# Kernel tuning notes

Measured on AMD Instinct MI355X. Metric: run time of the kernel, lower is better.

Reference implementation:

```python
import jax, jax.numpy as jnp
import numpy as np
from jax import lax

B, L, D_MODEL = 4, 1024, 512
D_STATE, D_CONV, D_INNER = 16, 4, 2 * D_MODEL


def setup_inputs() -> dict:
    key = jax.random.key(0)
    ks = jax.random.split(key, 8)
    s = 0.02
    x = jax.random.normal(ks[0], (B, L, D_MODEL), dtype=jnp.float32)
    W_in = jax.random.normal(ks[1], (D_MODEL, 2 * D_INNER), dtype=jnp.float32) * s
    conv_w = jax.random.normal(ks[2], (D_INNER, 1, D_CONV), dtype=jnp.float32) * s  # OIH, depthwise
    conv_b = jnp.zeros((D_INNER,), jnp.float32)
    W_x = jax.random.normal(ks[3], (D_INNER, 2 * D_STATE), dtype=jnp.float32) * s
    W_dt = jax.random.normal(ks[4], (D_INNER, D_INNER), dtype=jnp.float32) * s
    b_dt = jnp.zeros((D_INNER,), jnp.float32)
    # A_log = -logspace(log10(0.001), log10(1.0), d_state); used directly as A in the scan
    A_log = -jnp.logspace(np.log10(1e-3), 0.0, D_STATE, dtype=jnp.float32)
    D_skip = jnp.ones((D_INNER,), jnp.float32) * 0.1
    W_out = jax.random.normal(ks[5], (D_INNER, D_MODEL), dtype=jnp.float32) * s
    gamma = jnp.ones((D_MODEL,), jnp.float32)
    beta = jnp.zeros((D_MODEL,), jnp.float32)
    return dict(x=x, W_in=W_in, conv_w=conv_w, conv_b=conv_b, W_x=W_x, W_dt=W_dt,
                b_dt=b_dt, A_log=A_log, D_skip=D_skip, W_out=W_out, gamma=gamma, beta=beta)


def _mamba_forward(x, W_in, conv_w, conv_b, W_x, W_dt, b_dt, A_log, D_skip, W_out, gamma, beta):
    x = jnp.clip(x, -10.0, 10.0)
    x_and_res = x @ W_in                                  # [B, L, 2*d_inner]
    xp, res = jnp.split(x_and_res, 2, axis=-1)
    # Depthwise causal conv1d: torch pads d_conv-1 both sides then slices [:L] -> left-pad only.
    xt = jnp.transpose(xp, (0, 2, 1))                     # [B, d_inner, L]
    xc = lax.conv_general_dilated(xt, conv_w, window_strides=(1,),
                                  padding=[(D_CONV - 1, 0)],
                                  dimension_numbers=('NCH', 'OIH', 'NCH'),
                                  feature_group_count=D_INNER)
    xc = xc + conv_b[None, :, None]
    xc = jax.nn.silu(jnp.transpose(xc, (0, 2, 1)))        # [B, L, d_inner]
    ssm = xc @ W_x                                        # [B, L, 2*d_state]
    Bm, Cm = jnp.split(ssm, 2, axis=-1)                   # each [B, L, d_state]
    delta = xc @ W_dt + b_dt                              # [B, L, d_inner] (no softplus in source)

    # Selective scan over time (sequential recurrence)
    def step(h, inp):
        u_t, d_t, B_t, C_t = inp                          # [B,I], [B,I], [B,S], [B,S]
        dA = jnp.exp(jnp.clip(d_t[:, :, None] * A_log, -5.0, 5.0))   # [B, I, S]
        h = dA * h + (d_t[:, :, None] * B_t[:, None, :]) * u_t[:, :, None]
        y = jnp.einsum('bis,bs->bi', h, C_t)
        return h, y

    tm = lambda a: jnp.swapaxes(a, 0, 1)                  # time-major
    h0 = jnp.zeros((x.shape[0], D_INNER, D_STATE), xc.dtype)
    _, ys = lax.scan(step, h0, (tm(xc), tm(delta), tm(Bm), tm(Cm)))
    y = jnp.swapaxes(ys, 0, 1) + xc * D_skip              # D skip connection

    y = y * jax.nn.silu(res)                              # gating
    out = y @ W_out
    r = out + x                                           # residual
    mu = jnp.mean(r, axis=-1, keepdims=True)
    var = jnp.var(r, axis=-1, keepdims=True)
    return gamma * (r - mu) / jnp.sqrt(var + 1e-5) + beta


def reference(x, W_in, conv_w, conv_b, W_x, W_dt, b_dt, A_log, D_skip, W_out, gamma, beta):
    return _mamba_forward(x, W_in, conv_w, conv_b, W_x, W_dt, b_dt, A_log, D_skip, W_out, gamma, beta)
```

## Files before the change

kernel.cpp:

```cpp
#include <hip/hip_runtime.h>
#include <hip/hip_bf16.h>

typedef __hip_bfloat16 bf16;
typedef unsigned short ushort_t;
typedef unsigned int uint_t;
typedef __attribute__((ext_vector_type(8))) __bf16 bf16x8;
typedef __attribute__((ext_vector_type(8))) ushort_t u16x8;
typedef __attribute__((ext_vector_type(4))) ushort_t u16x4;
typedef __attribute__((ext_vector_type(4))) float f32x4;

#define BB 4
#define LL 1024
#define DM 512
#define DS 16
#define DI 1024
#define ROWS 4096
#define NC 64
#define CT 16

__device__ __forceinline__ float b2f(bf16 v) { return __bfloat162float(v); }

__device__ __forceinline__ float load_flag(const void* src, int i, int isbf)
{
    return isbf ? b2f(((const bf16*)src)[i]) : ((const float*)src)[i];
}

__device__ __forceinline__ ushort_t f2b_bits(float v)
{
    bf16 t = __float2bfloat16(v);
    return *(ushort_t*)&t;
}

__device__ __forceinline__ float bits2f(ushort_t u)
{
    uint_t w = ((uint_t)u) << 16;
    return __uint_as_float(w);
}

__device__ __forceinline__ int detect_local(const ushort_t* wdt)
{
    __shared__ int bad;
    if (threadIdx.x == 0) bad = 0;
    __syncthreads();
    ushort_t u = wdt[threadIdx.x & 255];
    if (((u >> 7) & 0xFF) >= 127) atomicAdd(&bad, 1);
    __syncthreads();
    return (bad <= 8) ? 1 : 0;
}

__global__ __launch_bounds__(256)
void prep_all(const void* x, const void* Win, const void* Wdt, const void* Wx,
              const void* Wout, const void* cw, const void* cb, const void* Alog,
              const void* Dsk, const void* gam, const void* bet, const void* bdtin,
              bf16* __restrict__ xbf, bf16* __restrict__ WtIn,
              bf16* __restrict__ WtDt, bf16* __restrict__ WtSsm,
              bf16* __restrict__ WtOut,
              float* __restrict__ ccw, float* __restrict__ ccb,
              float* __restrict__ cAlg, float* __restrict__ cDsk,
              float* __restrict__ cgam, float* __restrict__ cbet,
              float* __restrict__ bdt)
{
    const int isbf = detect_local((const ushort_t*)Wdt);
    int blk = blockIdx.x;

    if (blk < 2048) {
        int idx = blk * 256 + threadIdx.x;
        float v[4];
        if (isbf) {
            uint2 raw = ((const uint2*)x)[idx];
            v[0] = __uint_as_float(raw.x << 16);
            v[1] = __uint_as_float(raw.x & 0xFFFF0000u);
            v[2] = __uint_as_float(raw.y << 16);
            v[3] = __uint_as_float(raw.y & 0xFFFF0000u);
        } else {
            float4 raw = ((const float4*)x)[idx];
            v[0] = raw.x; v[1] = raw.y; v[2] = raw.z; v[3] = raw.w;
        }
        uint_t b0, b1;
        b0 = f2b_bits(fminf(fmaxf(v[0], -10.f), 10.f))
           | ((uint_t)f2b_bits(fminf(fmaxf(v[1], -10.f), 10.f)) << 16);
        b1 = f2b_bits(fminf(fmaxf(v[2], -10.f), 10.f))
           | ((uint_t)f2b_bits(fminf(fmaxf(v[3], -10.f), 10.f)) << 16);
        uint2 ow; ow.x = b0; ow.y = b1;
        ((uint2*)xbf)[idx] = ow;
    } else if (blk < 4640) {
        int tb = blk - 2048;
        const void* src; bf16* dst; int K, Nsrc, tpr;
        if (tb < 1024)      { src = Win;  dst = WtIn;  K = 512;  Nsrc = 2048; tpr = 64; }
        else if (tb < 2048) { tb -= 1024; src = Wdt;  dst = WtDt;  K = 1024; Nsrc = 1024; tpr = 32; }
        else if (tb < 2080) { tb -= 2048; src = Wx;   dst = WtSsm; K = 1024; Nsrc = 32;   tpr = 1; }
        else                { tb -= 2080; src = Wout; dst = WtOut; K = 1024; Nsrc = 512;  tpr = 16; }
        int k0 = (tb / tpr) * 32, n0 = (tb % tpr) * 32;

        __shared__ float tile[32][33];
        int tx = threadIdx.x & 31, ty = threadIdx.x >> 5;
        #pragma unroll
        for (int j = 0; j < 4; ++j)
            tile[ty + 8 * j][tx] = load_flag(src, (k0 + ty + 8 * j) * Nsrc + n0 + tx, isbf);
        __syncthreads();
        #pragma unroll
        for (int j = 0; j < 4; ++j)
            dst[(size_t)(n0 + ty + 8 * j) * K + k0 + tx] = __float2bfloat16(tile[tx][ty + 8 * j]);
    } else {
        int i = (blk - 4640) * 256 + threadIdx.x;
        if (i < 4096)        ccw[i] = load_flag(cw, i, isbf);
        else if (i < 5120)   ccb[i - 4096] = load_flag(cb, i - 4096, isbf);
        else if (i < 5136)   cAlg[i - 5120] = load_flag(Alog, i - 5120, isbf);
        else if (i < 6160)   cDsk[i - 5136] = load_flag(Dsk, i - 5136, isbf);
        else if (i < 6672)   cgam[i - 6160] = load_flag(gam, i - 6160, isbf);
        else if (i < 7184)   cbet[i - 6672] = load_flag(bet, i - 6672, isbf);
        else if (i < 8208)   bdt[i - 7184] = load_flag(bdtin, i - 7184, isbf);
        else if (i < 40976)  (WtSsm + 32 * 1024)[i - 8208] = __float2bfloat16(0.f);
    }
}

__device__ __forceinline__ void gload16(const bf16* g, ushort_t* l)
{
    __builtin_amdgcn_global_load_lds(
        (const __attribute__((address_space(1))) void*)g,
        (__attribute__((address_space(3))) void*)l, 16, 0, 0);
}

template <int TM, int TN, bool OBF, bool OT>
__global__ __launch_bounds__(256)
void gemm_mfma(const bf16* __restrict__ A, const bf16* __restrict__ Bt,
               const float* __restrict__ bias, void* __restrict__ Cv,
               int M, int N, int K)
{
    constexpr int MI = TM / 32, NJ = TN / 32;
    constexpr int NQA = TM * 8 / 256;
    constexpr int NQB = TN * 8 / 256;
    __shared__ ushort_t As[TM * 64];
    __shared__ ushort_t Bs[TN * 64];

    const int tid = threadIdx.x;
    const int lane = tid & 63;
    const int w = tid >> 6;
    const int wr = w >> 1, wc = w & 1;
    const int m0 = blockIdx.y * TM;
    const int n0 = blockIdx.x * TN;

    const bf16* gA[NQA]; ushort_t* lA[NQA];
    #pragma unroll
    for (int q = 0; q < NQA; ++q) {
        int p = q * 256 + tid;
        int row = p >> 3, kc = ((p & 7) - row) & 7;
        gA[q] = A + (size_t)(m0 + row) * K + kc * 8;
        lA[q] = &As[(q * 256 + w * 64) * 8];
    }
    const bf16* gB[NQB]; ushort_t* lB[NQB];
    #pragma unroll
    for (int q = 0; q < NQB; ++q) {
        int p = q * 256 + tid;
        int row = p >> 3, kc = ((p & 7) - row) & 7;
        gB[q] = Bt + (size_t)(n0 + row) * K + kc * 8;
        lB[q] = &Bs[(q * 256 + w * 64) * 8];
    }

    f32x4 acc[MI][NJ];
    #pragma unroll
    for (int i = 0; i < MI; ++i)
        #pragma unroll
        for (int j = 0; j < NJ; ++j)
            acc[i][j] = (f32x4){0.f, 0.f, 0.f, 0.f};

    const int ko = lane >> 4;
    const int ml = lane & 15;

    for (int k0 = 0; k0 < K; k0 += 64) {
        #pragma unroll
        for (int q = 0; q < NQA; ++q) gload16(gA[q] + k0, lA[q]);
        #pragma unroll
        for (int q = 0; q < NQB; ++q) gload16(gB[q] + k0, lB[q]);
        __syncthreads();

        #pragma unroll
        for (int half = 0; half < 2; ++half) {
            bf16x8 af[MI], bfr[NJ];
            #pragma unroll
            for (int i = 0; i < MI; ++i) {
                int m = wr * (TM / 2) + i * 16 + ml;
                af[i] = *(const bf16x8*)&As[(m * 8 + ((half * 4 + ko + m) & 7)) * 8];
            }
            #pragma unroll
            for (int j = 0; j < NJ; ++j) {
                int n = wc * (TN / 2) + j * 16 + ml;
                bfr[j] = *(const bf16x8*)&Bs[(n * 8 + ((half * 4 + ko + n) & 7)) * 8];
            }
            #pragma unroll
            for (int i = 0; i < MI; ++i)
                #pragma unroll
                for (int j = 0; j < NJ; ++j)
                    acc[i][j] = __builtin_amdgcn_mfma_f32_16x16x32_bf16(
                        af[i], bfr[j], acc[i][j], 0, 0, 0);
        }
        __syncthreads();
    }

    const int rq = lane >> 4;
    #pragma unroll
    for (int j = 0; j < NJ; ++j) {
        int n = n0 + wc * (TN / 2) + j * 16 + ml;
        float bv = bias ? bias[n] : 0.f;
        #pragma unroll
        for (int i = 0; i < MI; ++i) {
            int mb = m0 + wr * (TM / 2) + i * 16 + rq * 4;
            if (OT) {
                u16x4 pk;
                #pragma unroll
                for (int r = 0; r < 4; ++r)
                    pk[r] = f2b_bits(acc[i][j][r] + bv);
                *(u16x4*)((ushort_t*)Cv + (size_t)n * M + mb) = pk;
            } else {
                #pragma unroll
                for (int r = 0; r < 4; ++r) {
                    float v = acc[i][j][r] + bv;
                    if (OBF) ((bf16*)Cv)[(size_t)(mb + r) * N + n] = __float2bfloat16(v);
                    else     ((float*)Cv)[(size_t)(mb + r) * N + n] = v;
                }
            }
        }
    }
}

__global__ __launch_bounds__(256)
void conv_silu(const bf16* __restrict__ xrbT, const float* __restrict__ cw,
               const float* __restrict__ cb, bf16* __restrict__ xcT,
               bf16* __restrict__ xc)
{
    __shared__ ushort_t tile[64 * 72];
    const int blk = blockIdx.x;
    const int ch0 = (blk & 15) * 64;
    const int T0b = (blk >> 4) * 64;
    const int lc = threadIdx.x >> 2, tg = threadIdx.x & 3;
    const int i = ch0 + lc;
    const int T0 = T0b + tg * 16;

    const ushort_t* base = (const ushort_t*)xrbT + (size_t)i * ROWS + T0;
    u16x8 m0 = *(const u16x8*)base;
    u16x8 m1 = *(const u16x8*)(base + 8);
    u16x8 pv = {0, 0, 0, 0, 0, 0, 0, 0};
    if ((T0 & (LL - 1)) != 0) pv = *(const u16x8*)(base - 8);

    float4 w = ((const float4*)cw)[i];
    float bs = cb[i];
    float xm3 = bits2f(pv[5]), xm2 = bits2f(pv[6]), xm1 = bits2f(pv[7]);
    u16x8 o0, o1;
    #pragma unroll
    for (int tt = 0; tt < 16; ++tt) {
        float x0 = bits2f(tt < 8 ? m0[tt] : m1[tt - 8]);
        float acc = bs;
        acc = fmaf(xm3, w.x, acc);
        acc = fmaf(xm2, w.y, acc);
        acc = fmaf(xm1, w.z, acc);
        acc = fmaf(x0,  w.w, acc);
        ushort_t ob = f2b_bits(acc / (1.f + __expf(-acc)));
        if (tt < 8) o0[tt] = ob; else o1[tt - 8] = ob;
        xm3 = xm2; xm2 = xm1; xm1 = x0;
    }
    ushort_t* dt = (ushort_t*)xcT + (size_t)i * ROWS + T0;
    *(u16x8*)dt = o0;
    *(u16x8*)(dt + 8) = o1;
    *(u16x8*)&tile[lc * 72 + tg * 16] = o0;
    *(u16x8*)&tile[lc * 72 + tg * 16 + 8] = o1;
    __syncthreads();
    const int lt = threadIdx.x >> 2, cg = threadIdx.x & 3;
    u16x8 q0, q1;
    #pragma unroll
    for (int j = 0; j < 8; ++j) q0[j] = tile[(cg * 16 + j) * 72 + lt];
    #pragma unroll
    for (int j = 8; j < 16; ++j) q1[j - 8] = tile[(cg * 16 + j) * 72 + lt];
    ushort_t* wp = (ushort_t*)xc + (size_t)(T0b + lt) * DI + ch0 + cg * 16;
    *(u16x8*)wp = q0;
    *(u16x8*)(wp + 8) = q1;
}

__global__ __launch_bounds__(1024)
void scan_fused(const bf16* __restrict__ xcT, const bf16* __restrict__ dT,
                const bf16* __restrict__ ssm, const bf16* __restrict__ xrbT,
                const float* __restrict__ A_log, const float* __restrict__ Dskip,
                bf16* __restrict__ ybf)
{
    __shared__ uint_t lsum[DS * NC * 16];

    const int tid = threadIdx.x;
    const int b = blockIdx.x >> 6;
    const int ch0 = (blockIdx.x & 63) << 4;
    const int chl = tid & 15;
    const int c = tid >> 4;
    const int i = ch0 + chl;
    const size_t tb = (size_t)b * LL + c * CT;

    float a[DS];
    #pragma unroll
    for (int s = 0; s < DS; ++s) {
        uint_t bits = (uint_t)__builtin_amdgcn_readfirstlane((int)__float_as_uint(A_log[s]));
        a[s] = __uint_as_float(bits);
    }

    const u16x8* dp = (const u16x8*)((const ushort_t*)dT + (size_t)i * ROWS + tb);
    const u16x8* up = (const u16x8*)((const ushort_t*)xcT + (size_t)i * ROWS + tb);
    const u16x8* rp = (const u16x8*)((const ushort_t*)xrbT + (size_t)(1024 + i) * ROWS + tb);

    float h[DS] = {};
    float p[DS];
    #pragma unroll
    for (int s = 0; s < DS; ++s) p[s] = 1.f;

    #pragma unroll
    for (int half = 0; half < 2; ++half) {
        u16x8 dv8 = dp[half];
        u16x8 uv8 = up[half];
        #pragma unroll
        for (int t = 0; t < 8; ++t) {
            float dv = bits2f(dv8[t]);
            float uv = bits2f(uv8[t]);
            float du = dv * uv;
            const u16x8* sp = (const u16x8*)((const ushort_t*)ssm + (tb + half * 8 + t) * 64);
            u16x8 B0 = sp[0], B1 = sp[1];
            #pragma unroll
            for (int s = 0; s < DS; ++s) {
                float e = fminf(fmaxf(dv * a[s], -5.f), 5.f);
                float dA = __expf(e);
                float Bv = bits2f(s < 8 ? B0[s] : B1[s - 8]);
                h[s] = fmaf(dA, h[s], du * Bv);
                p[s] *= dA;
            }
        }
    }
    #pragma unroll
    for (int s = 0; s < DS; ++s)
        lsum[s * 1024 + tid] = (uint_t)f2b_bits(p[s]) | ((uint_t)f2b_bits(h[s]) << 16);
    __syncthreads();

    if (tid < 256) {
        int cl = tid & 15, s = tid >> 4;
        float hh = 0.f;
        for (int cc = 0; cc < NC; ++cc) {
            int off = s * 1024 + cc * 16 + cl;
            uint_t wrd = lsum[off];
            float pp = bits2f((ushort_t)(wrd & 0xFFFF));
            float qq = bits2f((ushort_t)(wrd >> 16));
            lsum[off] = (uint_t)f2b_bits(hh);
            hh = fmaf(pp, hh, qq);
        }
    }
    __syncthreads();

    #pragma unroll
    for (int s = 0; s < DS; ++s) h[s] = bits2f((ushort_t)lsum[s * 1024 + tid]);

    const float dsk = Dskip[i];

    #pragma unroll
    for (int half = 0; half < 2; ++half) {
        u16x8 dv8 = dp[half];
        u16x8 uv8 = up[half];
        u16x8 rv8 = rp[half];
        #pragma unroll
        for (int t = 0; t < 8; ++t) {
            float dv = bits2f(dv8[t]);
            float uv = bits2f(uv8[t]);
            float du = dv * uv;
            const u16x8* sp = (const u16x8*)((const ushort_t*)ssm + (tb + half * 8 + t) * 64);
            u16x8 B0 = sp[0], B1 = sp[1], C0 = sp[2], C1 = sp[3];
            float y = 0.f;
            #pragma unroll
            for (int s = 0; s < DS; ++s) {
                float e = fminf(fmaxf(dv * a[s], -5.f), 5.f);
                float dA = __expf(e);
                float Bv = bits2f(s < 8 ? B0[s] : B1[s - 8]);
                float Cc = bits2f(s < 8 ? C0[s] : C1[s - 8]);
                h[s] = fmaf(dA, h[s], du * Bv);
                y = fmaf(h[s], Cc, y);
            }
            float res = bits2f(rv8[t]);
            float g = res / (1.f + __expf(-res));
            ybf[(tb + half * 8 + t) * DI + i] = __float2bfloat16((y + uv * dsk) * g);
        }
    }
}

__global__ __launch_bounds__(256)
void ln_kernel(const float* __restrict__ outp, const void* __restrict__ xsrc,
               const void* __restrict__ wdt_probe,
               const float* __restrict__ gamma, const float* __restrict__ beta,
               void* __restrict__ out)
{
    const int isbf = detect_local((const ushort_t*)wdt_probe);
    const int row = blockIdx.x;
    const int tid = threadIdx.x;

    float r[2];
    float sum = 0.f, ss = 0.f;
    #pragma unroll
    for (int q = 0; q < 2; ++q) {
        int j = tid + q * 256;
        float xv = load_flag(xsrc, row * DM + j, isbf);
        xv = fminf(fmaxf(xv, -10.f), 10.f);
        float v = outp[(size_t)row * DM + j] + xv;
        r[q] = v;
        sum += v;
        ss = fmaf(v, v, ss);
    }
    #pragma unroll
    for (int off = 32; off >= 1; off >>= 1) {
        sum += __shfl_down(sum, off);
        ss  += __shfl_down(ss, off);
    }
    __shared__ float s1[4], s2[4];
    __shared__ float stats[2];
    int wid = tid >> 6, lane = tid & 63;
    if (lane == 0) { s1[wid] = sum; s2[wid] = ss; }
    __syncthreads();
    if (tid == 0) {
        float S = s1[0] + s1[1] + s1[2] + s1[3];
        float Qq = s2[0] + s2[1] + s2[2] + s2[3];
        float mean = S / DM;
        float var = Qq / DM - mean * mean;
        stats[0] = mean;
        stats[1] = rsqrtf(var + 1e-5f);
    }
    __syncthreads();
    float mean = stats[0], rstd = stats[1];
    #pragma unroll
    for (int q = 0; q < 2; ++q) {
        int j = tid + q * 256;
        float v = (r[q] - mean) * rstd * gamma[j] + beta[j];
        size_t o = (size_t)row * DM + j;
        if (isbf) ((bf16*)out)[o] = __float2bfloat16(v);
        else      ((float*)out)[o] = v;
    }
}

extern "C" void kernel_launch(void* const* d_in, const int* in_sizes, int n_in,
                              void* d_out, int out_size, void* d_ws, size_t ws_size,
                              hipStream_t stream)
{
    float* W = (float*)d_ws;
    float* ccw  = W;
    float* ccb  = ccw  + 4096;
    float* cAlg = ccb  + 1024;
    float* cDsk = cAlg + 16;
    float* cgam = cDsk + 1024;
    float* cbet = cgam + 512;
    float* bdt  = cbet + 512;
    float* outp = bdt  + 1024;
    bf16*  xbf  = (bf16*)(outp + 2097152);
    bf16*  xrbT = xbf  + 2097152;
    bf16*  xcT  = xrbT + 8388608;
    bf16*  xc   = xcT  + 4194304;
    bf16*  ybf  = xc   + 4194304;
    bf16*  dT   = ybf  + 4194304;
    bf16*  ssm  = dT   + 4194304;
    bf16*  WtIn = ssm  + 262144;
    bf16*  WtDt = WtIn + 1048576;
    bf16*  WtSsm= WtDt + 1048576;
    bf16*  WtOut= WtSsm+ 65536;

    prep_all<<<4801, 256, 0, stream>>>(
        d_in[0], d_in[1], d_in[5], d_in[4], d_in[9], d_in[2], d_in[3],
        d_in[7], d_in[8], d_in[10], d_in[11], d_in[6],
        xbf, WtIn, WtDt, WtSsm, WtOut, ccw, ccb, cAlg, cDsk, cgam, cbet, bdt);

    gemm_mfma<64, 128, true, true><<<dim3(2048 / 128, ROWS / 64), 256, 0, stream>>>(
        xbf, WtIn, nullptr, xrbT, ROWS, 2048, 512);

    conv_silu<<<1024, 256, 0, stream>>>(xrbT, ccw, ccb, xcT, xc);

    gemm_mfma<64, 128, true, true><<<dim3(DI / 128, ROWS / 64), 256, 0, stream>>>(
        xc, WtDt, bdt, dT, ROWS, DI, DI);

    gemm_mfma<32, 64, true, false><<<dim3(1, ROWS / 32), 256, 0, stream>>>(
        xc, WtSsm, nullptr, ssm, ROWS, 64, DI);

    scan_fused<<<256, 1024, 0, stream>>>(xcT, dT, ssm, xrbT, cAlg, cDsk, ybf);

    gemm_mfma<64, 64, false, false><<<dim3(DM / 64, ROWS / 64), 256, 0, stream>>>(
        ybf, WtOut, nullptr, outp, ROWS, DM, DI);

    ln_kernel<<<ROWS, 256, 0, stream>>>(outp, d_in[0], d_in[5], cgam, cbet, d_out);
}
```

Baseline: 216.9 us.

## Fuse delta and B/C projections into one GEMM, rechunk scan, bf16 out-proj

Concatenates the W_dt and W_x weight matrices, padded to 1152 columns, so one GEMM produces delta (transposed) and the B/C projections. A split epilogue routes the extra columns to the ssm buffer, which removes a separate narrow, poorly occupied GEMM launch. The chunked scan now uses 128 chunks of 8 timesteps and 8 channels per block, doubling the block count to 512 for more parallelism. The cost is a longer cross-chunk combine in LDS. The output projection writes bf16 instead of fp32 to halve traffic into layernorm, which adds rounding error.

```diff
diff --git a/kernel.cpp b/kernel.cpp
--- a/kernel.cpp
+++ b/kernel.cpp
@@ -15,8 +15,10 @@
 #define DS 16
 #define DI 1024
 #define ROWS 4096
-#define NC 64
-#define CT 16
+#define NC 128
+#define CT 8
+#define NCH 8
+#define NDTX 1152
 
 __device__ __forceinline__ float b2f(bf16 v) { return __bfloat162float(v); }
 
@@ -53,12 +55,11 @@
               const void* Wout, const void* cw, const void* cb, const void* Alog,
               const void* Dsk, const void* gam, const void* bet, const void* bdtin,
               bf16* __restrict__ xbf, bf16* __restrict__ WtIn,
-              bf16* __restrict__ WtDt, bf16* __restrict__ WtSsm,
-              bf16* __restrict__ WtOut,
+              bf16* __restrict__ WtDtx, bf16* __restrict__ WtOut,
               float* __restrict__ ccw, float* __restrict__ ccb,
               float* __restrict__ cAlg, float* __restrict__ cDsk,
               float* __restrict__ cgam, float* __restrict__ cbet,
-              float* __restrict__ bdt)
+              float* __restrict__ bdtx)
 {
     const int isbf = detect_local((const ushort_t*)Wdt);
     int blk = blockIdx.x;
@@ -86,10 +87,10 @@
     } else if (blk < 4640) {
         int tb = blk - 2048;
         const void* src; bf16* dst; int K, Nsrc, tpr;
-        if (tb < 1024)      { src = Win;  dst = WtIn;  K = 512;  Nsrc = 2048; tpr = 64; }
-        else if (tb < 2048) { tb -= 1024; src = Wdt;  dst = WtDt;  K = 1024; Nsrc = 1024; tpr = 32; }
-        else if (tb < 2080) { tb -= 2048; src = Wx;   dst = WtSsm; K = 1024; Nsrc = 32;   tpr = 1; }
-        else                { tb -= 2080; src = Wout; dst = WtOut; K = 1024; Nsrc = 512;  tpr = 16; }
+        if (tb < 1024)      { src = Win;  dst = WtIn;   K = 512;  Nsrc = 2048; tpr = 64; }
+        else if (tb < 2048) { tb -= 1024; src = Wdt;  dst = WtDtx; K = 1024; Nsrc = 1024; tpr = 32; }
+        else if (tb < 2080) { tb -= 2048; src = Wx;   dst = WtDtx + 1024 * 1024; K = 1024; Nsrc = 32; tpr = 1; }
+        else                { tb -= 2080; src = Wout; dst = WtOut;  K = 1024; Nsrc = 512;  tpr = 16; }
         int k0 = (tb / tpr) * 32, n0 = (tb % tpr) * 32;
 
         __shared__ float tile[32][33];
@@ -109,8 +110,12 @@
         else if (i < 6160)   cDsk[i - 5136] = load_flag(Dsk, i - 5136, isbf);
         else if (i < 6672)   cgam[i - 6160] = load_flag(gam, i - 6160, isbf);
         else if (i < 7184)   cbet[i - 6672] = load_flag(bet, i - 6672, isbf);
-        else if (i < 8208)   bdt[i - 7184] = load_flag(bdtin, i - 7184, isbf);
-        else if (i < 40976)  (WtSsm + 32 * 1024)[i - 8208] = __float2bfloat16(0.f);
+        else if (i < 8336) {
+            int j = i - 7184;
+            bdtx[j] = (j < DI) ? load_flag(bdtin, j, isbf) : 0.f;
+        } else if (i < 106640) {
+            (WtDtx + 1056 * 1024)[i - 8336] = __float2bfloat16(0.f);
+        }
     }
 }
 
@@ -121,11 +126,11 @@
         (__attribute__((address_space(3))) void*)l, 16, 0, 0);
 }
 
-template <int TM, int TN, bool OBF, bool OT>
+template <int TM, int TN, bool OBF, bool OT, bool SPLIT>
 __global__ __launch_bounds__(256)
 void gemm_mfma(const bf16* __restrict__ A, const bf16* __restrict__ Bt,
                const float* __restrict__ bias, void* __restrict__ Cv,
-               int M, int N, int K)
+               void* __restrict__ Cv2, int M, int N, int K)
 {
     constexpr int MI = TM / 32, NJ = TN / 32;
     constexpr int NQA = TM * 8 / 256;
@@ -205,7 +210,14 @@
         #pragma unroll
         for (int i = 0; i < MI; ++i) {
             int mb = m0 + wr * (TM / 2) + i * 16 + rq * 4;
-            if (OT) {
+            if (SPLIT && n >= 1024) {
+                if (n < 1088) {
+                    #pragma unroll
+                    for (int r = 0; r < 4; ++r)
+                        ((bf16*)Cv2)[(size_t)(mb + r) * 64 + (n - 1024)] =
+                            __float2bfloat16(acc[i][j][r] + bv);
+                }
+            } else if (OT) {
                 u16x4 pk;
                 #pragma unroll
                 for (int r = 0; r < 4; ++r)
@@ -281,13 +293,13 @@
                 const float* __restrict__ A_log, const float* __restrict__ Dskip,
                 bf16* __restrict__ ybf)
 {
-    __shared__ uint_t lsum[DS * NC * 16];
+    __shared__ uint_t lsum[DS * NC * NCH];
 
     const int tid = threadIdx.x;
-    const int b = blockIdx.x >> 6;
-    const int ch0 = (blockIdx.x & 63) << 4;
-    const int chl = tid & 15;
-    const int c = tid >> 4;
+    const int b = blockIdx.x >> 7;
+    const int ch0 = (blockIdx.x & 127) << 3;
+    const int chl = tid & 7;
+    const int c = tid >> 3;
     const int i = ch0 + chl;
     const size_t tb = (size_t)b * LL + c * CT;
 
@@ -307,16 +319,15 @@
     #pragma unroll
     for (int s = 0; s < DS; ++s) p[s] = 1.f;
 
-    #pragma unroll
-    for (int half = 0; half < 2; ++half) {
-        u16x8 dv8 = dp[half];
-        u16x8 uv8 = up[half];
-        #pragma unroll
-        for (int t = 0; t < 8; ++t) {
+    {
+        u16x8 dv8 = dp[0];
+        u16x8 uv8 = up[0];
+        #pragma unroll
+        for (int t = 0; t < CT; ++t) {
             float dv = bits2f(dv8[t]);
             float uv = bits2f(uv8[t]);
             float du = dv * uv;
-            const u16x8* sp = (const u16x8*)((const ushort_t*)ssm + (tb + half * 8 + t) * 64);
+            const u16x8* sp = (const u16x8*)((const ushort_t*)ssm + (tb + t) * 64);
             u16x8 B0 = sp[0], B1 = sp[1];
             #pragma unroll
             for (int s = 0; s < DS; ++s) {
@@ -330,14 +341,14 @@
     }
     #pragma unroll
     for (int s = 0; s < DS; ++s)
-        lsum[s * 1024 + tid] = (uint_t)f2b_bits(p[s]) | ((uint_t)f2b_bits(h[s]) << 16);
-    __syncthreads();
-
-    if (tid < 256) {
-        int cl = tid & 15, s = tid >> 4;
+        lsum[s * (NC * NCH) + tid] = (uint_t)f2b_bits(p[s]) | ((uint_t)f2b_bits(h[s]) << 16);
+    __syncthreads();
+
+    if (tid < NCH * DS) {
+        int cl = tid & 7, s = tid >> 3;
         float hh = 0.f;
         for (int cc = 0; cc < NC; ++cc) {
-            int off = s * 1024 + cc * 16 + cl;
+            int off = s * (NC * NCH) + cc * NCH + cl;
             uint_t wrd = lsum[off];
             float pp = bits2f((ushort_t)(wrd & 0xFFFF));
             float qq = bits2f((ushort_t)(wrd >> 16));
@@ -348,21 +359,20 @@
     __syncthreads();
 
     #pragma unroll
-    for (int s = 0; s < DS; ++s) h[s] = bits2f((ushort_t)lsum[s * 1024 + tid]);
+    for (int s = 0; s < DS; ++s) h[s] = bits2f((ushort_t)lsum[s * (NC * NCH) + tid]);
 
     const float dsk = Dskip[i];
 
-    #pragma unroll
-    for (int half = 0; half < 2; ++half) {
-        u16x8 dv8 = dp[half];
-        u16x8 uv8 = up[half];
-        u16x8 rv8 = rp[half];
-        #pragma unroll
-        for (int t = 0; t < 8; ++t) {
+    {
+        u16x8 dv8 = dp[0];
+        u16x8 uv8 = up[0];
+        u16x8 rv8 = rp[0];
+        #pragma unroll
+        for (int t = 0; t < CT; ++t) {
             float dv = bits2f(dv8[t]);
             float uv = bits2f(uv8[t]);
             float du = dv * uv;
-            const u16x8* sp = (const u16x8*)((const ushort_t*)ssm + (tb + half * 8 + t) * 64);
+            const u16x8* sp = (const u16x8*)((const ushort_t*)ssm + (tb + t) * 64);
             u16x8 B0 = sp[0], B1 = sp[1], C0 = sp[2], C1 = sp[3];
             float y = 0.f;
             #pragma unroll
@@ -376,13 +386,13 @@
             }
             float res = bits2f(rv8[t]);
             float g = res / (1.f + __expf(-res));
-            ybf[(tb + half * 8 + t) * DI + i] = __float2bfloat16((y + uv * dsk) * g);
+            ybf[(tb + t) * DI + i] = __float2bfloat16((y + uv * dsk) * g);
         }
     }
 }
 
 __global__ __launch_bounds__(256)
-void ln_kernel(const float* __restrict__ outp, const void* __restrict__ xsrc,
+void ln_kernel(const bf16* __restrict__ outp, const void* __restrict__ xsrc,
                const void* __restrict__ wdt_probe,
                const float* __restrict__ gamma, const float* __restrict__ beta,
                void* __restrict__ out)
@@ -398,7 +408,7 @@
         int j = tid + q * 256;
         float xv = load_flag(xsrc, row * DM + j, isbf);
         xv = fminf(fmaxf(xv, -10.f), 10.f);
-        float v = outp[(size_t)row * DM + j] + xv;
+        float v = b2f(outp[(size_t)row * DM + j]) + xv;
         r[q] = v;
         sum += v;
         ss = fmaf(v, v, ss);
@@ -444,40 +454,36 @@
     float* cDsk = cAlg + 16;
     float* cgam = cDsk + 1024;
     float* cbet = cgam + 512;
-    float* bdt  = cbet + 512;
-    float* outp = bdt  + 1024;
-    bf16*  xbf  = (bf16*)(outp + 2097152);
+    float* bdtx = cbet + 512;
+    bf16*  xbf  = (bf16*)(bdtx + 1152);
     bf16*  xrbT = xbf  + 2097152;
     bf16*  xcT  = xrbT + 8388608;
     bf16*  xc   = xcT  + 4194304;
     bf16*  ybf  = xc   + 4194304;
     bf16*  dT   = ybf  + 4194304;
     bf16*  ssm  = dT   + 4194304;
-    bf16*  WtIn = ssm  + 262144;
-    bf16*  WtDt = WtIn + 1048576;
-    bf16*  WtSsm= WtDt + 1048576;
-    bf16*  WtOut= WtSsm+ 65536;
-
-    prep_all<<<4801, 256, 0, stream>>>(
+    bf16*  outp = ssm  + 262144;
+    bf16*  WtIn = outp + 2097152;
+    bf16*  WtDtx= WtIn + 1048576;
+    bf16*  WtOut= WtDtx+ 1179648;
+
+    prep_all<<<5057, 256, 0, stream>>>(
         d_in[0], d_in[1], d_in[5], d_in[4], d_in[9], d_in[2], d_in[3],
         d_in[7], d_in[8], d_in[10], d_in[11], d_in[6],
-        xbf, WtIn, WtDt, WtSsm, WtOut, ccw, ccb, cAlg, cDsk, cgam, cbet, bdt);
-
-    gemm_mfma<64, 128, true, true><<<dim3(2048 / 128, ROWS / 64), 256, 0, stream>>>(
-        xbf, WtIn, nullptr, xrbT, ROWS, 2048, 512);
+        xbf, WtIn, WtDtx, WtOut, ccw, ccb, cAlg, cDsk, cgam, cbet, bdtx);
+
+    gemm_mfma<64, 128, true, true, false><<<dim3(2048 / 128, ROWS / 64), 256, 0, stream>>>(
+        xbf, WtIn, nullptr, xrbT, nullptr, ROWS, 2048, 512);
 
     conv_silu<<<1024, 256, 0, stream>>>(xrbT, ccw, ccb, xcT, xc);
 
-    gemm_mfma<64, 128, true, true><<<dim3(DI / 128, ROWS / 64), 256, 0, stream>>>(
-        xc, WtDt, bdt, dT, ROWS, DI, DI);
-
-    gemm_mfma<32, 64, true, false><<<dim3(1, ROWS / 32), 256, 0, stream>>>(
-        xc, WtSsm, nullptr, ssm, ROWS, 64, DI);
-
-    scan_fused<<<256, 1024, 0, stream>>>(xcT, dT, ssm, xrbT, cAlg, cDsk, ybf);
-
-    gemm_mfma<64, 64, false, false><<<dim3(DM / 64, ROWS / 64), 256, 0, stream>>>(
-        ybf, WtOut, nullptr, outp, ROWS, DM, DI);
+    gemm_mfma<64, 128, true, true, true><<<dim3(NDTX / 128, ROWS / 64), 256, 0, stream>>>(
+        xc, WtDtx, bdtx, dT, ssm, ROWS, NDTX, DI);
+
+    scan_fused<<<512, 1024, 0, stream>>>(xcT, dT, ssm, xrbT, cAlg, cDsk, ybf);
+
+    gemm_mfma<64, 64, true, false, false><<<dim3(DM / 64, ROWS / 64), 256, 0, stream>>>(
+        ybf, WtOut, nullptr, outp, nullptr, ROWS, DM, DI);
 
     ln_kernel<<<ROWS, 256, 0, stream>>>(outp, d_in[0], d_in[5], cgam, cbet, d_out);
 }
```

New measurement: 219.7 us. About the same (+1.2%).
